# Kernel optimization log

Measured on AMD Instinct MI355X. Metric: run time of the kernel, lower is better.

The kernel has to match this reference:

```python
import jax, jax.numpy as jnp
import numpy as np

K_DIM = 128

def setup_inputs() -> dict:
    key = jax.random.key(0)
    k1, k2, k3, k4 = jax.random.split(key, 4)
    B, S, D = 4, 4096, 1024
    input_vec = jax.random.normal(k1, (B, S, D), dtype=jnp.float32)
    # 'normal' Keras initializer ~ RandomNormal(stddev=0.05)
    weight_query = jax.random.normal(k2, (D, K_DIM), dtype=jnp.float32) * 0.05
    weight_key = jax.random.normal(k3, (D, K_DIM), dtype=jnp.float32) * 0.05
    weight_value = jax.random.normal(k4, (D, K_DIM), dtype=jnp.float32) * 0.05
    return {"input_vec": input_vec, "weight_query": weight_query,
            "weight_key": weight_key, "weight_value": weight_value}

def reference(input_vec, weight_query, weight_key, weight_value):
    # Q/K/V projections: [B,S,D] @ [D,K] -> [B,S,K]
    q = jnp.einsum('bsd,dk->bsk', input_vec, weight_query)
    k = jnp.einsum('bsd,dk->bsk', input_vec, weight_key)
    v = jnp.einsum('bsd,dk->bsk', input_vec, weight_value)
    scale = 1.0 / jnp.sqrt(jnp.asarray(K_DIM, dtype=q.dtype))
    # full score matrix [B,S,S], softmax over last axis (keys)
    scores = jnp.einsum('bqk,bsk->bqs', q, k) * scale
    attn = jax.nn.softmax(scores, axis=-1)
    return jnp.einsum('bqs,bsk->bqk', attn, v)
```

## Files before the change

kernel.cpp:

```cpp
#include <hip/hip_runtime.h>
#include <hip/hip_bf16.h>
#include <math.h>

#define B_  4
#define S_  4096
#define D_  1024
#define KD_ 128

typedef __attribute__((ext_vector_type(8))) short short8;
typedef __attribute__((ext_vector_type(4))) float f32x4;
typedef __attribute__((ext_vector_type(16))) float f32x16;
typedef __attribute__((ext_vector_type(4))) unsigned short us4;
typedef __attribute__((ext_vector_type(4))) unsigned int u32x4;

__device__ __forceinline__ unsigned short f2bf(float f) {
    __hip_bfloat16 h = __float2bfloat16(f);
    return *reinterpret_cast<unsigned short*>(&h);
}

__device__ __forceinline__ f32x4 mfma_bf16(short8 a, short8 b, f32x4 c) {
    return __builtin_amdgcn_mfma_f32_16x16x32_bf16(a, b, c, 0, 0, 0);
}

__device__ __forceinline__ f32x16 mfma32_bf16(short8 a, short8 b, f32x16 c) {
    return __builtin_amdgcn_mfma_f32_32x32x16_bf16(a, b, c, 0, 0, 0);
}

__device__ __forceinline__ unsigned int cvt_pk_bf16(float lo, float hi_) {
    unsigned int r;
    asm("v_cvt_pk_bf16_f32 %0, %1, %2" : "=v"(r) : "v"(lo), "v"(hi_));
    return r;
}

__device__ __forceinline__ void g2l16(const void* g, void* l) {
    __builtin_amdgcn_global_load_lds(
        (const __attribute__((address_space(1))) unsigned int*)g,
        (__attribute__((address_space(3))) unsigned int*)l, 16, 0, 0);
}

__global__ void convert_w_kernel(const float* __restrict__ wq,
                                 const float* __restrict__ wk,
                                 const float* __restrict__ wv,
                                 unsigned short* __restrict__ wt) {
    int t = blockIdx.x * 256 + threadIdx.x;
    int w = t >> 14;
    int r = t & 16383;
    int n = r & 127;
    int k8 = r >> 7;
    const float* src = (w == 0) ? wq : (w == 1) ? wk : wv;
    float scale = (w == 0) ? 0.12751725551033443f : 1.0f;
    short8 v;
#pragma unroll
    for (int i = 0; i < 8; ++i)
        v[i] = (short)f2bf(src[(size_t)(k8 * 8 + i) * KD_ + n] * scale);
    *reinterpret_cast<short8*>(&wt[(size_t)w * KD_ * D_ + (size_t)n * D_ + k8 * 8]) = v;
}

__global__ __launch_bounds__(256) void proj_kernel(
        const float* __restrict__ X, const unsigned short* __restrict__ Wt,
        unsigned short* __restrict__ Qo, unsigned short* __restrict__ Ko,
        unsigned short* __restrict__ Vt) {
    const int mtile = blockIdx.x;
    const int which = blockIdx.y;
    const int m0 = mtile * 128;
    const int tid = threadIdx.x;
    const int lane = tid & 63;
    const int wid = tid >> 6;
    const int wr = wid >> 1, wc = wid & 1;
    const int l15 = lane & 15, l4 = lane >> 4;

    __shared__ __align__(16) unsigned short Asm[128 * 64];
    __shared__ __align__(16) unsigned short Bsm[128 * 64];
    __shared__ __align__(16) unsigned short Tsm[128 * 128];

    const unsigned short* W = Wt + (size_t)which * KD_ * D_;

    f32x4 acc[4][4];
#pragma unroll
    for (int r = 0; r < 4; ++r)
#pragma unroll
        for (int c = 0; c < 4; ++c) acc[r][c] = (f32x4)0.0f;

    for (int k0 = 0; k0 < D_; k0 += 64) {
#pragma unroll
        for (int i = 0; i < 8; ++i) {
            int f = tid + i * 256;
            int row = f >> 4, c4 = f & 15;
            float4 xv = *reinterpret_cast<const float4*>(
                &X[(size_t)(m0 + row) * D_ + k0 + c4 * 4]);
            us4 h;
            h.x = f2bf(xv.x); h.y = f2bf(xv.y); h.z = f2bf(xv.z); h.w = f2bf(xv.w);
            *reinterpret_cast<us4*>(&Asm[row * 64 + c4 * 4]) = h;
        }
#pragma unroll
        for (int i = 0; i < 4; ++i) {
            int g = tid + i * 256;
            int n = g >> 3, c8 = g & 7;
            *reinterpret_cast<short8*>(&Bsm[n * 64 + c8 * 8]) =
                *reinterpret_cast<const short8*>(&W[(size_t)n * D_ + k0 + c8 * 8]);
        }
        __syncthreads();

        short8 a[4][2], b[4][2];
#pragma unroll
        for (int rt = 0; rt < 4; ++rt)
#pragma unroll
            for (int kc = 0; kc < 2; ++kc)
                a[rt][kc] = *reinterpret_cast<const short8*>(
                    &Asm[(wr * 64 + rt * 16 + l15) * 64 + kc * 32 + l4 * 8]);
#pragma unroll
        for (int ct = 0; ct < 4; ++ct)
#pragma unroll
            for (int kc = 0; kc < 2; ++kc)
                b[ct][kc] = *reinterpret_cast<const short8*>(
                    &Bsm[(wc * 64 + ct * 16 + l15) * 64 + kc * 32 + l4 * 8]);
#pragma unroll
        for (int kc = 0; kc < 2; ++kc)
#pragma unroll
            for (int rt = 0; rt < 4; ++rt)
#pragma unroll
                for (int ct = 0; ct < 4; ++ct)
                    acc[rt][ct] = mfma_bf16(a[rt][kc], b[ct][kc], acc[rt][ct]);
        __syncthreads();
    }

    if (which < 2) {
        unsigned short* O = (which == 0) ? Qo : Ko;
#pragma unroll
        for (int rt = 0; rt < 4; ++rt)
#pragma unroll
            for (int ct = 0; ct < 4; ++ct)
#pragma unroll
                for (int j = 0; j < 4; ++j) {
                    int row = m0 + wr * 64 + rt * 16 + l4 * 4 + j;
                    int col = wc * 64 + ct * 16 + l15;
                    O[(size_t)row * KD_ + col] = f2bf(acc[rt][ct][j]);
                }
    } else {
#pragma unroll
        for (int rt = 0; rt < 4; ++rt)
#pragma unroll
            for (int ct = 0; ct < 4; ++ct)
#pragma unroll
                for (int j = 0; j < 4; ++j) {
                    int row = wr * 64 + rt * 16 + l4 * 4 + j;
                    int col = wc * 64 + ct * 16 + l15;
                    Tsm[col * 128 + row] = f2bf(acc[rt][ct][j]);
                }
        __syncthreads();
        int bb = m0 >> 12;
        int s0 = m0 & 4095;
#pragma unroll
        for (int i = 0; i < 8; ++i) {
            int g = tid + i * 256;
            int n = g >> 4, s8 = g & 15;
            *reinterpret_cast<short8*>(
                &Vt[(size_t)bb * KD_ * S_ + (size_t)n * S_ + s0 + s8 * 8]) =
                *reinterpret_cast<short8*>(&Tsm[n * 128 + s8 * 8]);
        }
    }
}

__global__ __launch_bounds__(128, 2) void attn_split_kernel(
        const unsigned short* __restrict__ Q,
        const unsigned short* __restrict__ Kb,
        const unsigned short* __restrict__ Vt,
        float* __restrict__ part, float* __restrict__ lsumP) {
    const int bid = blockIdx.x;
    const int b  = bid & 3;
    const int s  = (bid >> 2) & 3;
    const int qt = bid >> 4;
    const int tid = threadIdx.x;
    const int lane = tid & 63;
    const int wg  = tid >> 6;
    const int q0 = qt * 64;
    const int l31 = lane & 31;
    const int hi  = lane >> 5;

    __shared__ __align__(16) unsigned short Ksm[2][32 * 128];
    __shared__ __align__(16) unsigned short Vsm[2][128 * 32];

    short8 aq[8];
    {
        const unsigned short* qrow =
            Q + ((size_t)(b * S_ + q0 + wg * 32 + l31)) * KD_;
#pragma unroll
        for (int kc = 0; kc < 8; ++kc)
            aq[kc] = *reinterpret_cast<const short8*>(&qrow[kc * 16 + hi * 8]);
    }

    f32x16 o[4];
#pragma unroll
    for (int dt = 0; dt < 4; ++dt) o[dt] = (f32x16)0.0f;
    float lsum = 0.0f;

    const unsigned short* Kbase = Kb + (size_t)b * S_ * KD_;
    const unsigned short* Vbase = Vt + (size_t)b * KD_ * S_;

    auto STAGE = [&](int buf, int kt) {
#pragma unroll
        for (int i = 0; i < 4; ++i) {
            int d = i * 128 + wg * 64 + lane;
            int row = d >> 4, c = d & 15;
            g2l16(&Kbase[(size_t)(kt * 32 + row) * KD_ + ((c ^ (row & 7)) * 8)],
                  &Ksm[buf][(i * 128 + wg * 64) * 8]);
        }
#pragma unroll
        for (int i = 0; i < 4; ++i) {
            int d = i * 128 + wg * 64 + lane;
            int row = d >> 2, c = d & 3;
            g2l16(&Vbase[(size_t)row * S_ + kt * 32 + ((c ^ ((row >> 1) & 3)) * 8)],
                  &Vsm[buf][(i * 128 + wg * 64) * 8]);
        }
    };

    int cur = 0;
    STAGE(0, s * 32);
    __syncthreads();

    for (int it = 0; it < 32; ++it) {
        if (it < 31) STAGE(cur ^ 1, s * 32 + it + 1);

        const unsigned short* ksm = &Ksm[cur][0];
        const unsigned short* vsm = &Vsm[cur][0];

        f32x16 sf = (f32x16)0.0f;
        __builtin_amdgcn_s_setprio(1);
#pragma unroll
        for (int kc = 0; kc < 8; ++kc) {
            short8 bk = *reinterpret_cast<const short8*>(
                &ksm[l31 * 128 + (((kc * 2 + hi) ^ (l31 & 7)) * 8)]);
            sf = mfma32_bf16(bk, aq[kc], sf);
        }
        __builtin_amdgcn_s_setprio(0);

        float p[16];
#pragma unroll
        for (int r = 0; r < 16; ++r) {
            p[r] = exp2f(sf[r]);
            lsum += p[r];
        }

        short8 pa[2];
#pragma unroll
        for (int c = 0; c < 2; ++c) {
            u32x4 wv;
#pragma unroll
            for (int e = 0; e < 2; ++e) {
                unsigned int X = cvt_pk_bf16(p[8 * c + 2 * e], p[8 * c + 2 * e + 1]);
                unsigned int Y = cvt_pk_bf16(p[8 * c + 4 + 2 * e], p[8 * c + 4 + 2 * e + 1]);
                unsigned int S = hi ? X : Y;
                unsigned int T = __shfl_xor(S, 32);
                wv[e]     = hi ? T : X;
                wv[2 + e] = hi ? Y : T;
            }
            pa[c] = __builtin_bit_cast(short8, wv);
        }

        __builtin_amdgcn_s_setprio(1);
#pragma unroll
        for (int c = 0; c < 2; ++c)
#pragma unroll
            for (int dt = 0; dt < 4; ++dt) {
                int row = dt * 32 + l31;
                short8 bv = *reinterpret_cast<const short8*>(
                    &vsm[row * 32 + (((c * 2 + hi) ^ ((row >> 1) & 3)) * 8)]);
                o[dt] = mfma32_bf16(pa[c], bv, o[dt]);
            }
        __builtin_amdgcn_s_setprio(0);

        __syncthreads();
        cur ^= 1;
    }

    lsum += __shfl_xor(lsum, 32);

    const int tile = (qt << 2) | b;
    float* Po = part + ((size_t)tile * 4 + s) * 8192;
#pragma unroll
    for (int r = 0; r < 16; ++r) {
        int row = wg * 32 + (r & 3) + 8 * (r >> 2) + 4 * hi;
#pragma unroll
        for (int dt = 0; dt < 4; ++dt)
            Po[row * 128 + dt * 32 + l31] = o[dt][r];
    }
    if (hi == 0)
        lsumP[((size_t)tile * 4 + s) * 64 + wg * 32 + l31] = lsum;
}

__global__ __launch_bounds__(256) void merge_kernel(
        const float* __restrict__ part, const float* __restrict__ lsumP,
        float* __restrict__ Out) {
    const int tile = blockIdx.x;
    const int b = tile & 3, qt = tile >> 2;
    const int tid = threadIdx.x;
    __shared__ float inv[64];
    if (tid < 64) {
        const float* lp = lsumP + (size_t)tile * 256;
        inv[tid] = 1.0f / (lp[tid] + lp[64 + tid] + lp[128 + tid] + lp[192 + tid]);
    }
    __syncthreads();
    const float* p = part + (size_t)tile * 4 * 8192;
    float* Ob = Out + ((size_t)b * S_ + qt * 64) * KD_;
#pragma unroll
    for (int i = 0; i < 8; ++i) {
        int idx = tid + i * 256;
        int row = idx >> 5;
        float4 v0 = *reinterpret_cast<const float4*>(&p[idx * 4]);
        float4 v1 = *reinterpret_cast<const float4*>(&p[8192 + idx * 4]);
        float4 v2 = *reinterpret_cast<const float4*>(&p[16384 + idx * 4]);
        float4 v3 = *reinterpret_cast<const float4*>(&p[24576 + idx * 4]);
        float iv = inv[row];
        float4 r;
        r.x = (v0.x + v1.x + v2.x + v3.x) * iv;
        r.y = (v0.y + v1.y + v2.y + v3.y) * iv;
        r.z = (v0.z + v1.z + v2.z + v3.z) * iv;
        r.w = (v0.w + v1.w + v2.w + v3.w) * iv;
        *reinterpret_cast<float4*>(&Ob[idx * 4]) = r;
    }
}

__global__ __launch_bounds__(512, 2) void attn_kernel(
        const unsigned short* __restrict__ Q,
        const unsigned short* __restrict__ Kb,
        const unsigned short* __restrict__ Vt,
        float* __restrict__ Out) {
    const int bid = blockIdx.x;
    const int b  = bid & 3;
    const int qt = bid >> 2;
    const int tid = threadIdx.x;
    const int lane = tid & 63;
    const int wid = tid >> 6;
    const int grp = wid >> 1;
    const int wg  = wid & 1;
    const int q0 = qt * 64;
    const int l31 = lane & 31;
    const int hi  = lane >> 5;

    __shared__ __align__(16) unsigned char lds_raw[131072];
    unsigned short* KsmA = (unsigned short*)lds_raw;
    unsigned short* VsmA = (unsigned short*)(lds_raw + 65536);

    short8 aq[8];
    {
        const unsigned short* qrow =
            Q + ((size_t)(b * S_ + q0 + wg * 32 + l31)) * KD_;
#pragma unroll
        for (int kc = 0; kc < 8; ++kc)
            aq[kc] = *reinterpret_cast<const short8*>(&qrow[kc * 16 + hi * 8]);
    }

    f32x16 o[4];
#pragma unroll
    for (int dt = 0; dt < 4; ++dt) o[dt] = (f32x16)0.0f;
    float lsum = 0.0f;

    const unsigned short* Kbase = Kb + (size_t)b * S_ * KD_;
    const unsigned short* Vbase = Vt + (size_t)b * KD_ * S_;

    unsigned short* Kgrp = KsmA + grp * 2 * 4096;
    unsigned short* Vgrp = VsmA + grp * 2 * 4096;

    auto STAGE = [&](int buf, int kt) {
#pragma unroll
        for (int i = 0; i < 4; ++i) {
            int d = i * 128 + wg * 64 + lane;
            int row = d >> 4, c = d & 15;
            g2l16(&Kbase[(size_t)(kt * 32 + row) * KD_ + ((c ^ (row & 7)) * 8)],
                  &Kgrp[(buf * 512 + i * 128 + wg * 64) * 8]);
        }
#pragma unroll
        for (int i = 0; i < 4; ++i) {
            int d = i * 128 + wg * 64 + lane;
            int row = d >> 2, c = d & 3;
            g2l16(&Vbase[(size_t)row * S_ + kt * 32 + ((c ^ ((row >> 1) & 3)) * 8)],
                  &Vgrp[(buf * 512 + i * 128 + wg * 64) * 8]);
        }
    };

    int cur = 0;
    STAGE(0, grp);
    __syncthreads();

    for (int it = 0; it < 32; ++it) {
        if (it < 31) STAGE(cur ^ 1, (it + 1) * 4 + grp);

        const unsigned short* ksm = Kgrp + cur * 4096;
        const unsigned short* vsm = Vgrp + cur * 4096;

        f32x16 sf = (f32x16)0.0f;
        __builtin_amdgcn_s_setprio(1);
#pragma unroll
        for (int kc = 0; kc < 8; ++kc) {
            short8 bk = *reinterpret_cast<const short8*>(
                &ksm[l31 * 128 + (((kc * 2 + hi) ^ (l31 & 7)) * 8)]);
            sf = mfma32_bf16(bk, aq[kc], sf);
        }
        __builtin_amdgcn_s_setprio(0);

        float p[16];
#pragma unroll
        for (int r = 0; r < 16; ++r) {
            p[r] = exp2f(sf[r]);
            lsum += p[r];
        }

        short8 pa[2];
#pragma unroll
        for (int c = 0; c < 2; ++c) {
            u32x4 wv;
#pragma unroll
            for (int e = 0; e < 2; ++e) {
                unsigned int X = cvt_pk_bf16(p[8 * c + 2 * e], p[8 * c + 2 * e + 1]);
                unsigned int Y = cvt_pk_bf16(p[8 * c + 4 + 2 * e], p[8 * c + 4 + 2 * e + 1]);
                unsigned int S = hi ? X : Y;
                unsigned int T = __shfl_xor(S, 32);
                wv[e]     = hi ? T : X;
                wv[2 + e] = hi ? Y : T;
            }
            pa[c] = __builtin_bit_cast(short8, wv);
        }

        __builtin_amdgcn_s_setprio(1);
#pragma unroll
        for (int c = 0; c < 2; ++c)
#pragma unroll
            for (int dt = 0; dt < 4; ++dt) {
                int row = dt * 32 + l31;
                short8 bv = *reinterpret_cast<const short8*>(
                    &vsm[row * 32 + (((c * 2 + hi) ^ ((row >> 1) & 3)) * 8)]);
                o[dt] = mfma32_bf16(pa[c], bv, o[dt]);
            }
        __builtin_amdgcn_s_setprio(0);

        __syncthreads();
        cur ^= 1;
    }

    lsum += __shfl_xor(lsum, 32);

    float* scratch = (float*)lds_raw;
    float* lsumS   = (float*)(lds_raw + 98304);
    __syncthreads();
    if (grp >= 1) {
        int base = (grp - 1) * 8192;
#pragma unroll
        for (int dt = 0; dt < 4; ++dt)
#pragma unroll
            for (int r = 0; r < 16; ++r) {
                int row = wg * 32 + (r & 3) + 8 * (r >> 2) + 4 * hi;
                scratch[base + row * 128 + dt * 32 + l31] = o[dt][r];
            }
    }
    if (hi == 0) lsumS[grp * 64 + wg * 32 + l31] = lsum;
    __syncthreads();
    if (grp == 0) {
        float* Ob = Out + (size_t)b * S_ * KD_;
#pragma unroll
        for (int r = 0; r < 16; ++r) {
            int row = wg * 32 + (r & 3) + 8 * (r >> 2) + 4 * hi;
            float inv = 1.0f / (lsumS[row] + lsumS[64 + row] +
                                lsumS[128 + row] + lsumS[192 + row]);
#pragma unroll
            for (int dt = 0; dt < 4; ++dt) {
                int col = dt * 32 + l31;
                int idx = row * 128 + col;
                float v = o[dt][r] + scratch[idx] + scratch[8192 + idx] +
                          scratch[16384 + idx];
                Ob[(size_t)(q0 + row) * KD_ + col] = v * inv;
            }
        }
    }
}

extern "C" void kernel_launch(void* const* d_in, const int* in_sizes, int n_in,
                              void* d_out, int out_size, void* d_ws, size_t ws_size,
                              hipStream_t stream) {
    const float* X  = (const float*)d_in[0];
    const float* Wq = (const float*)d_in[1];
    const float* Wk = (const float*)d_in[2];
    const float* Wv = (const float*)d_in[3];
    float* Out = (float*)d_out;

    unsigned short* Wt  = (unsigned short*)d_ws;
    unsigned short* Q16 = (unsigned short*)((char*)d_ws + 786432);
    unsigned short* K16 = Q16 + (size_t)16384 * 128;
    unsigned short* V16 = K16 + (size_t)16384 * 128;
    float* part  = (float*)((char*)d_ws + 13369344);
    float* lsumP = (float*)((char*)d_ws + 46923776);
    const size_t ws_need = 47185920;

    hipLaunchKernelGGL(convert_w_kernel, dim3(192), dim3(256), 0, stream,
                       Wq, Wk, Wv, Wt);
    hipLaunchKernelGGL(proj_kernel, dim3(128, 3), dim3(256), 0, stream,
                       X, Wt, Q16, K16, V16);
    if (ws_size >= ws_need) {
        hipLaunchKernelGGL(attn_split_kernel, dim3(1024), dim3(128), 0, stream,
                           Q16, K16, V16, part, lsumP);
        hipLaunchKernelGGL(merge_kernel, dim3(256), dim3(256), 0, stream,
                           part, lsumP, Out);
    } else {
        hipLaunchKernelGGL(attn_kernel, dim3(256), dim3(512), 0, stream,
                           Q16, K16, V16, Out);
    }
}
```

Baseline: 105.2 us.

## Split keys eight ways with bf16 partials and regroup projection blocks

Raises the key-axis split of the attention kernel from 4 to 8, giving 2048 blocks of 16 iterations each, and stores the partial outputs as bf16 instead of fp32. The merge kernel now sums 8 bf16 partials. The projection grid is flattened so the three Q/K/V blocks that share an X tile run close together, which should improve L2 reuse of X. The row-sum accumulation is split across two accumulators. The aim is better occupancy and less partial-buffer traffic, at the cost of bf16 rounding on the partial sums.

Measured after the change: 118.0 us. 1.12x slower.

```diff
diff --git a/kernel.cpp b/kernel.cpp
--- a/kernel.cpp
+++ b/kernel.cpp
@@ -6,6 +6,9 @@
 #define S_  4096
 #define D_  1024
 #define KD_ 128
+#define NSPL 8
+#define SPAN (S_ / NSPL)
+#define NIT  (SPAN / 32)
 
 typedef __attribute__((ext_vector_type(8))) short short8;
 typedef __attribute__((ext_vector_type(4))) float f32x4;
@@ -60,8 +63,11 @@
         const float* __restrict__ X, const unsigned short* __restrict__ Wt,
         unsigned short* __restrict__ Qo, unsigned short* __restrict__ Ko,
         unsigned short* __restrict__ Vt) {
-    const int mtile = blockIdx.x;
-    const int which = blockIdx.y;
+    const int bid = blockIdx.x;
+    const int g = bid / 24;
+    const int local = bid - g * 24;
+    const int which = local >> 3;
+    const int mtile = g * 8 + (local & 7);
     const int m0 = mtile * 128;
     const int tid = threadIdx.x;
     const int lane = tid & 63;
@@ -94,8 +100,8 @@
         }
 #pragma unroll
         for (int i = 0; i < 4; ++i) {
-            int g = tid + i * 256;
-            int n = g >> 3, c8 = g & 7;
+            int gg = tid + i * 256;
+            int n = gg >> 3, c8 = gg & 7;
             *reinterpret_cast<short8*>(&Bsm[n * 64 + c8 * 8]) =
                 *reinterpret_cast<const short8*>(&W[(size_t)n * D_ + k0 + c8 * 8]);
         }
@@ -152,8 +158,8 @@
         int s0 = m0 & 4095;
 #pragma unroll
         for (int i = 0; i < 8; ++i) {
-            int g = tid + i * 256;
-            int n = g >> 4, s8 = g & 15;
+            int gg = tid + i * 256;
+            int n = gg >> 4, s8 = gg & 15;
             *reinterpret_cast<short8*>(
                 &Vt[(size_t)bb * KD_ * S_ + (size_t)n * S_ + s0 + s8 * 8]) =
                 *reinterpret_cast<short8*>(&Tsm[n * 128 + s8 * 8]);
@@ -165,11 +171,11 @@
         const unsigned short* __restrict__ Q,
         const unsigned short* __restrict__ Kb,
         const unsigned short* __restrict__ Vt,
-        float* __restrict__ part, float* __restrict__ lsumP) {
+        unsigned short* __restrict__ part16, float* __restrict__ lsumP) {
     const int bid = blockIdx.x;
     const int b  = bid & 3;
-    const int s  = (bid >> 2) & 3;
-    const int qt = bid >> 4;
+    const int s  = (bid >> 2) & 7;
+    const int qt = bid >> 5;
     const int tid = threadIdx.x;
     const int lane = tid & 63;
     const int wg  = tid >> 6;
@@ -192,7 +198,7 @@
     f32x16 o[4];
 #pragma unroll
     for (int dt = 0; dt < 4; ++dt) o[dt] = (f32x16)0.0f;
-    float lsum = 0.0f;
+    float lsA = 0.0f, lsB = 0.0f;
 
     const unsigned short* Kbase = Kb + (size_t)b * S_ * KD_;
     const unsigned short* Vbase = Vt + (size_t)b * KD_ * S_;
@@ -215,11 +221,11 @@
     };
 
     int cur = 0;
-    STAGE(0, s * 32);
+    STAGE(0, s * NIT);
     __syncthreads();
 
-    for (int it = 0; it < 32; ++it) {
-        if (it < 31) STAGE(cur ^ 1, s * 32 + it + 1);
+    for (int it = 0; it < NIT; ++it) {
+        if (it < NIT - 1) STAGE(cur ^ 1, s * NIT + it + 1);
 
         const unsigned short* ksm = &Ksm[cur][0];
         const unsigned short* vsm = &Vsm[cur][0];
@@ -238,7 +244,7 @@
 #pragma unroll
         for (int r = 0; r < 16; ++r) {
             p[r] = exp2f(sf[r]);
-            lsum += p[r];
+            if (r & 1) lsB += p[r]; else lsA += p[r];
         }
 
         short8 pa[2];
@@ -249,8 +255,8 @@
             for (int e = 0; e < 2; ++e) {
                 unsigned int X = cvt_pk_bf16(p[8 * c + 2 * e], p[8 * c + 2 * e + 1]);
                 unsigned int Y = cvt_pk_bf16(p[8 * c + 4 + 2 * e], p[8 * c + 4 + 2 * e + 1]);
-                unsigned int S = hi ? X : Y;
-                unsigned int T = __shfl_xor(S, 32);
+                unsigned int Ss = hi ? X : Y;
+                unsigned int T = __shfl_xor(Ss, 32);
                 wv[e]     = hi ? T : X;
                 wv[2 + e] = hi ? Y : T;
             }
@@ -273,50 +279,61 @@
         cur ^= 1;
     }
 
+    float lsum = lsA + lsB;
     lsum += __shfl_xor(lsum, 32);
 
     const int tile = (qt << 2) | b;
-    float* Po = part + ((size_t)tile * 4 + s) * 8192;
+    unsigned short* Po = part16 + ((size_t)tile * NSPL + s) * 8192;
 #pragma unroll
     for (int r = 0; r < 16; ++r) {
         int row = wg * 32 + (r & 3) + 8 * (r >> 2) + 4 * hi;
 #pragma unroll
         for (int dt = 0; dt < 4; ++dt)
-            Po[row * 128 + dt * 32 + l31] = o[dt][r];
+            Po[row * 128 + dt * 32 + l31] = f2bf(o[dt][r]);
     }
     if (hi == 0)
-        lsumP[((size_t)tile * 4 + s) * 64 + wg * 32 + l31] = lsum;
+        lsumP[((size_t)tile * NSPL + s) * 64 + wg * 32 + l31] = lsum;
 }
 
 __global__ __launch_bounds__(256) void merge_kernel(
-        const float* __restrict__ part, const float* __restrict__ lsumP,
-        float* __restrict__ Out) {
+        const unsigned short* __restrict__ part16,
+        const float* __restrict__ lsumP, float* __restrict__ Out) {
     const int tile = blockIdx.x;
     const int b = tile & 3, qt = tile >> 2;
     const int tid = threadIdx.x;
     __shared__ float inv[64];
     if (tid < 64) {
-        const float* lp = lsumP + (size_t)tile * 256;
-        inv[tid] = 1.0f / (lp[tid] + lp[64 + tid] + lp[128 + tid] + lp[192 + tid]);
+        const float* lp = lsumP + (size_t)tile * (NSPL * 64);
+        float t = 0.0f;
+#pragma unroll
+        for (int s = 0; s < NSPL; ++s) t += lp[s * 64 + tid];
+        inv[tid] = 1.0f / t;
     }
     __syncthreads();
-    const float* p = part + (size_t)tile * 4 * 8192;
+    const unsigned short* p = part16 + (size_t)tile * NSPL * 8192;
     float* Ob = Out + ((size_t)b * S_ + qt * 64) * KD_;
 #pragma unroll
-    for (int i = 0; i < 8; ++i) {
-        int idx = tid + i * 256;
-        int row = idx >> 5;
-        float4 v0 = *reinterpret_cast<const float4*>(&p[idx * 4]);
-        float4 v1 = *reinterpret_cast<const float4*>(&p[8192 + idx * 4]);
-        float4 v2 = *reinterpret_cast<const float4*>(&p[16384 + idx * 4]);
-        float4 v3 = *reinterpret_cast<const float4*>(&p[24576 + idx * 4]);
+    for (int i = 0; i < 4; ++i) {
+        int g = tid + i * 256;
+        int row = g >> 4;
+        float acc8[8] = {0, 0, 0, 0, 0, 0, 0, 0};
+#pragma unroll
+        for (int s = 0; s < NSPL; ++s) {
+            short8 v = *reinterpret_cast<const short8*>(&p[s * 8192 + g * 8]);
+#pragma unroll
+            for (int j = 0; j < 8; ++j) {
+                unsigned int u = ((unsigned int)(unsigned short)v[j]) << 16;
+                acc8[j] += __uint_as_float(u);
+            }
+        }
         float iv = inv[row];
-        float4 r;
-        r.x = (v0.x + v1.x + v2.x + v3.x) * iv;
-        r.y = (v0.y + v1.y + v2.y + v3.y) * iv;
-        r.z = (v0.z + v1.z + v2.z + v3.z) * iv;
-        r.w = (v0.w + v1.w + v2.w + v3.w) * iv;
-        *reinterpret_cast<float4*>(&Ob[idx * 4]) = r;
+        float4 r0, r1;
+        r0.x = acc8[0] * iv; r0.y = acc8[1] * iv;
+        r0.z = acc8[2] * iv; r0.w = acc8[3] * iv;
+        r1.x = acc8[4] * iv; r1.y = acc8[5] * iv;
+        r1.z = acc8[6] * iv; r1.w = acc8[7] * iv;
+        *reinterpret_cast<float4*>(&Ob[g * 8]) = r0;
+        *reinterpret_cast<float4*>(&Ob[g * 8 + 4]) = r1;
     }
 }
 
@@ -413,8 +430,8 @@
             for (int e = 0; e < 2; ++e) {
                 unsigned int X = cvt_pk_bf16(p[8 * c + 2 * e], p[8 * c + 2 * e + 1]);
                 unsigned int Y = cvt_pk_bf16(p[8 * c + 4 + 2 * e], p[8 * c + 4 + 2 * e + 1]);
-                unsigned int S = hi ? X : Y;
-                unsigned int T = __shfl_xor(S, 32);
+                unsigned int Ss = hi ? X : Y;
+                unsigned int T = __shfl_xor(Ss, 32);
                 wv[e]     = hi ? T : X;
                 wv[2 + e] = hi ? Y : T;
             }
@@ -486,19 +503,19 @@
     unsigned short* Q16 = (unsigned short*)((char*)d_ws + 786432);
     unsigned short* K16 = Q16 + (size_t)16384 * 128;
     unsigned short* V16 = K16 + (size_t)16384 * 128;
-    float* part  = (float*)((char*)d_ws + 13369344);
-    float* lsumP = (float*)((char*)d_ws + 46923776);
-    const size_t ws_need = 47185920;
+    unsigned short* part16 = (unsigned short*)((char*)d_ws + 13369344);
+    float* lsumP = (float*)((char*)d_ws + 13369344 + 33554432);
+    const size_t ws_need = 13369344 + 33554432 + 524288;
 
     hipLaunchKernelGGL(convert_w_kernel, dim3(192), dim3(256), 0, stream,
                        Wq, Wk, Wv, Wt);
-    hipLaunchKernelGGL(proj_kernel, dim3(128, 3), dim3(256), 0, stream,
+    hipLaunchKernelGGL(proj_kernel, dim3(384), dim3(256), 0, stream,
                        X, Wt, Q16, K16, V16);
     if (ws_size >= ws_need) {
-        hipLaunchKernelGGL(attn_split_kernel, dim3(1024), dim3(128), 0, stream,
-                           Q16, K16, V16, part, lsumP);
+        hipLaunchKernelGGL(attn_split_kernel, dim3(2048), dim3(128), 0, stream,
+                           Q16, K16, V16, part16, lsumP);
         hipLaunchKernelGGL(merge_kernel, dim3(256), dim3(256), 0, stream,
-                           part, lsumP, Out);
+                           part16, lsumP, Out);
     } else {
         hipLaunchKernelGGL(attn_kernel, dim3(256), dim3(512), 0, stream,
                            Q16, K16, V16, Out);
```
